# Performance work log

Hardware: AMD Instinct MI355X
Metric: run time of the kernel (lower is better)

The kernel has to match this reference:

```python
import jax, jax.numpy as jnp
import numpy as np

N, D, E = 16384, 256, 8
H = D // 2  # gate hidden


def setup_inputs() -> dict:
    key = jax.random.key(0)
    ks = jax.random.split(key, 10)
    s = lambda fan_in: 1.0 / np.sqrt(fan_in)
    return {
        "x":   jax.random.normal(ks[0], (N, D), dtype=jnp.float32),
        # gate: Linear(D, D//2) -> ReLU -> Linear(D//2, E) -> Softmax
        "Wg1": jax.random.uniform(ks[1], (D, H), jnp.float32, -s(D), s(D)),
        "bg1": jax.random.uniform(ks[2], (H,), jnp.float32, -s(D), s(D)),
        "Wg2": jax.random.uniform(ks[3], (H, E), jnp.float32, -s(H), s(H)),
        "bg2": jax.random.uniform(ks[4], (E,), jnp.float32, -s(H), s(H)),
        # experts: per-expert Linear(D,D) -> ReLU -> (Dropout eval=identity) -> Linear(D,D)
        "W1": jax.random.uniform(ks[5], (E, D, D), jnp.float32, -s(D), s(D)),
        "b1": jax.random.uniform(ks[6], (E, D), jnp.float32, -s(D), s(D)),
        "W2": jax.random.uniform(ks[7], (E, D, D), jnp.float32, -s(D), s(D)),
        "b2": jax.random.uniform(ks[8], (E, D), jnp.float32, -s(D), s(D)),
    }


def reference(x, Wg1, bg1, Wg2, bg2, W1, b1, W2, b2):
    # gate: [N, E] softmax over experts
    g = jax.nn.softmax(jax.nn.relu(x @ Wg1 + bg1) @ Wg2 + bg2, axis=-1)
    # all experts applied densely via batched GEMMs (fuses the Python loop)
    h = jax.nn.relu(jnp.einsum("nd,edh->neh", x, W1) + b1)  # [N, E, D]
    y = jnp.einsum("neh,ehd->ned", h, W2) + b2              # [N, E, D]
    # weighted combine: sum_e g[n,e] * y[n,e,:]
    return jnp.einsum("ned,ne->nd", y, g)
```

## Files before the change

kernel.cpp:

```cpp
#include <hip/hip_runtime.h>


typedef unsigned short USH;
typedef float f32x4 __attribute__((ext_vector_type(4)));
typedef __bf16 bf16x8 __attribute__((ext_vector_type(8)));

#define AS1 __attribute__((address_space(1)))
#define AS3 __attribute__((address_space(3)))

__device__ __forceinline__ USH f2bf(float f) {
  unsigned int u = __float_as_uint(f);
  u += 0x7fffu + ((u >> 16) & 1u);
  return (USH)(u >> 16);
}

__device__ __forceinline__ void gl2lds16(const void* g, void* l) {
  __builtin_amdgcn_global_load_lds((AS1 const void*)g, (AS3 void*)l, 16, 0, 0);
}


__global__ __launch_bounds__(256) void k_prep(
    const float* __restrict__ x,
    const float* __restrict__ Wg1,
    const float* __restrict__ W1,
    const float* __restrict__ W2,
    USH* __restrict__ xb, USH* __restrict__ wg1t,
    USH* __restrict__ w1f, USH* __restrict__ w2f) {
  __shared__ float T[64][65];
  int b = blockIdx.x, tid = threadIdx.x;

  if (b < 2048) {
    size_t i8 = ((size_t)b * 256 + tid) * 8;
    float4 a = *(const float4*)(x + i8);
    float4 c = *(const float4*)(x + i8 + 4);
    USH v[8];
    v[0] = f2bf(a.x); v[1] = f2bf(a.y); v[2] = f2bf(a.z); v[3] = f2bf(a.w);
    v[4] = f2bf(c.x); v[5] = f2bf(c.y); v[6] = f2bf(c.z); v[7] = f2bf(c.w);
    *(uint4*)(xb + i8) = *(const uint4*)v;
  } else if (b < 2176) {
    int bp = b - 2048;
    int e = bp >> 4, tl = bp & 15;
    int c0 = (tl >> 2) * 64, h0 = (tl & 3) * 64;
    const float* src = W1 + (size_t)e * 65536;
#pragma unroll
    for (int p = 0; p < 4; ++p) {
      int r = p * 16 + (tid >> 4), d4 = (tid & 15) * 4;
      float4 v = *(const float4*)(src + (size_t)(c0 + r) * 256 + h0 + d4);
      T[r][d4] = v.x; T[r][d4 + 1] = v.y; T[r][d4 + 2] = v.z; T[r][d4 + 3] = v.w;
    }
    __syncthreads();
#pragma unroll
    for (int p = 0; p < 4; ++p) {
      int hr = p * 16 + (tid >> 4), c4 = (tid & 15) * 4;
      USH w[4];
#pragma unroll
      for (int j = 0; j < 4; ++j) w[j] = f2bf(T[c4 + j][hr]);
      int h = h0 + hr;
      int t = h >> 4, lh = h & 15;
      int kt = c0 >> 6, ch = c4 >> 5, q = (c4 >> 3) & 3, u0 = c4 & 7;
      size_t idx = ((size_t)((e * 64 + kt * 16 + t) * 2 + ch)) * 512 + (q * 16 + lh) * 8 + u0;
      *(uint2*)(w1f + idx) = *(const uint2*)w;
    }
  } else if (b < 2184) {
    int bp = b - 2176;
    int c0 = (bp >> 1) * 64, h0 = (bp & 1) * 64;
#pragma unroll
    for (int p = 0; p < 4; ++p) {
      int r = p * 16 + (tid >> 4), d4 = (tid & 15) * 4;
      float4 v = *(const float4*)(Wg1 + (size_t)(c0 + r) * 128 + h0 + d4);
      T[r][d4] = v.x; T[r][d4 + 1] = v.y; T[r][d4 + 2] = v.z; T[r][d4 + 3] = v.w;
    }
    __syncthreads();
#pragma unroll
    for (int p = 0; p < 4; ++p) {
      int hr = p * 16 + (tid >> 4), c4 = (tid & 15) * 4;
      USH w[4];
#pragma unroll
      for (int j = 0; j < 4; ++j) w[j] = f2bf(T[c4 + j][hr]);
      *(uint2*)(wg1t + (size_t)(h0 + hr) * 256 + c0 + c4) = *(const uint2*)w;
    }
  } else {
    int bp = b - 2184;
    int e = bp >> 4, tl = bp & 15;
    int h0 = (tl >> 2) * 64, d0 = (tl & 3) * 64;
    const float* src = W2 + (size_t)e * 65536;
#pragma unroll
    for (int p = 0; p < 4; ++p) {
      int r = p * 16 + (tid >> 4), d4 = (tid & 15) * 4;
      float4 v = *(const float4*)(src + (size_t)(h0 + r) * 256 + d0 + d4);
      T[r][d4] = v.x; T[r][d4 + 1] = v.y; T[r][d4 + 2] = v.z; T[r][d4 + 3] = v.w;
    }
    __syncthreads();
#pragma unroll
    for (int p = 0; p < 4; ++p) {
      int dr = p * 16 + (tid >> 4), h4 = (tid & 15) * 4;
      USH w[4];
#pragma unroll
      for (int j = 0; j < 4; ++j) w[j] = f2bf(T[h4 + j][dr]);
      int d = d0 + dr;
      int t = d >> 4, ld = d & 15;
      int ht = h0 >> 6, ch = h4 >> 5, q = (h4 >> 3) & 3, u0 = h4 & 7;
      size_t idx = ((size_t)((e * 64 + ht * 16 + t) * 2 + ch)) * 512 + (q * 16 + ld) * 8 + u0;
      *(uint2*)(w2f + idx) = *(const uint2*)w;
    }
  }
}


__global__ __launch_bounds__(256) void k_gate(const USH* __restrict__ xb,
                                              const USH* __restrict__ wg1t,
                                              const float* __restrict__ bg1,
                                              const float* __restrict__ wg2,
                                              const float* __restrict__ bg2,
                                              float* __restrict__ g) {
  __shared__ __align__(16) USH As[32 * 64];
  __shared__ __align__(16) USH Bs[128 * 64];
  __shared__ float hg[32 * 129];
  __shared__ float bg1s[128];
  __shared__ float w2s[128 * 8];
  __shared__ float b2s[8];
  __shared__ float lg[32 * 8];

  int tid = threadIdx.x;
  int wave = tid >> 6, lane = tid & 63;
  int quad = lane >> 4, l16 = lane & 15;
  int sw = l16 & 7;
  int wr = wave >> 1, wc = wave & 1;
  int rowBase = blockIdx.x * 32;

  for (int t = tid; t < 1024; t += 256) w2s[t] = wg2[t];
  if (tid < 8) b2s[tid] = bg2[tid];
  if (tid < 128) bg1s[tid] = bg1[tid];

  f32x4 acc[4] = {};
  for (int kt = 0; kt < 4; ++kt) {
    int kb = kt * 64;
    {
      int r = tid >> 3, c8 = (tid & 7) ^ (r & 7);
      gl2lds16(xb + (size_t)(rowBase + r) * 256 + kb + c8 * 8, As + (size_t)tid * 8);
    }
#pragma unroll
    for (int c = 0; c < 4; ++c) {
      int i = c * 256 + tid;
      int r = i >> 3, c8 = (i & 7) ^ (r & 7);
      gl2lds16(wg1t + (size_t)r * 256 + kb + c8 * 8, Bs + (size_t)i * 8);
    }
    __syncthreads();
#pragma unroll
    for (int kkc = 0; kkc < 8; kkc += 4) {
      bf16x8 av = *(const bf16x8*)(As + (wr * 16 + l16) * 64 + (((kkc + quad) ^ sw) * 8));
#pragma unroll
      for (int j = 0; j < 4; ++j) {
        bf16x8 bv = *(const bf16x8*)(Bs + (wc * 64 + j * 16 + l16) * 64 + (((kkc + quad) ^ sw) * 8));
        acc[j] = __builtin_amdgcn_mfma_f32_16x16x32_bf16(av, bv, acc[j], 0, 0, 0);
      }
    }
    __syncthreads();
  }

#pragma unroll
  for (int j = 0; j < 4; ++j)
#pragma unroll
    for (int r = 0; r < 4; ++r) {
      int row = wr * 16 + quad * 4 + r;
      int col = wc * 64 + j * 16 + l16;
      hg[row * 129 + col] = fmaxf(acc[j][r] + bg1s[col], 0.0f);
    }
  __syncthreads();

  {
    int row = tid >> 3, p = tid & 7;
    float s = b2s[p];
    for (int k = 0; k < 128; ++k) s += hg[row * 129 + k] * w2s[k * 8 + p];
    lg[row * 8 + p] = s;
  }
  __syncthreads();

  if (tid < 32) {
    float l[8];
    float m = -1e30f;
#pragma unroll
    for (int e = 0; e < 8; ++e) { l[e] = lg[tid * 8 + e]; m = fmaxf(m, l[e]); }
    float s = 0.0f;
#pragma unroll
    for (int e = 0; e < 8; ++e) { l[e] = expf(l[e] - m); s += l[e]; }
    float inv = 1.0f / s;
    size_t grow = rowBase + tid;
#pragma unroll
    for (int e = 0; e < 8; ++e) g[grow * 8 + e] = l[e] * inv;
  }
}


__global__ __launch_bounds__(512, 2) void k_moe(const USH* __restrict__ xb,
                                                const USH* __restrict__ w1f,
                                                const USH* __restrict__ w2f,
                                                const float* __restrict__ b1,
                                                const float* __restrict__ b2,
                                                const float* __restrict__ g,
                                                float* __restrict__ out) {
  __shared__ __align__(16) USH Hs[64 * 256];
  __shared__ float b1s[2048];
  __shared__ float b2s[2048];
  __shared__ float gs[512];

  int tid = threadIdx.x;
  int wave = tid >> 6, lane = tid & 63;
  int quad = lane >> 4, l16 = lane & 15;
  int sw = l16 & 7;
  int rowBase = blockIdx.x * 64;

#pragma unroll
  for (int t = 0; t < 4; ++t) {
    b1s[t * 512 + tid] = b1[t * 512 + tid];
    b2s[t * 512 + tid] = b2[t * 512 + tid];
  }
  gs[tid] = g[(size_t)rowBase * 8 + tid];

  bf16x8 xr[4][2][4];
#pragma unroll
  for (int kt = 0; kt < 4; ++kt)
#pragma unroll
    for (int c = 0; c < 2; ++c)
#pragma unroll
      for (int j = 0; j < 4; ++j)
        xr[kt][c][j] = *(const bf16x8*)(xb + (size_t)(rowBase + j * 16 + l16) * 256 +
                                        kt * 64 + c * 32 + quad * 8);

  __syncthreads();

  f32x4 oacc[4][2] = {};

#pragma unroll 1
  for (int e = 0; e < 8; ++e) {
    const USH* W1e = w1f + (size_t)e * 65536;
    const USH* W2e = w2f + (size_t)e * 65536;
    f32x4 hacc[2][4] = {};

#pragma unroll
    for (int kt = 0; kt < 4; ++kt)
#pragma unroll
      for (int c = 0; c < 2; ++c) {
        bf16x8 av[2];
#pragma unroll
        for (int i = 0; i < 2; ++i)
          av[i] = *(const bf16x8*)(W1e + (size_t)((kt * 16 + wave * 2 + i) * 2 + c) * 512 + lane * 8);
#pragma unroll
        for (int i = 0; i < 2; ++i)
#pragma unroll
          for (int j = 0; j < 4; ++j)
            hacc[i][j] = __builtin_amdgcn_mfma_f32_16x16x32_bf16(av[i], xr[kt][c][j], hacc[i][j], 0, 0, 0);
      }

#pragma unroll
    for (int i = 0; i < 2; ++i) {
      int slot = (wave & 1) * 4 + i * 2 + (quad >> 1);
      int hb = wave * 32 + i * 16 + quad * 4;
#pragma unroll
      for (int j = 0; j < 4; ++j) {
        int n = j * 16 + l16;
        float gg = gs[n * 8 + e];
        USH w4[4];
#pragma unroll
        for (int r = 0; r < 4; ++r)
          w4[r] = f2bf(fmaxf(hacc[i][j][r] + b1s[e * 256 + hb + r], 0.0f) * gg);
        int off = n * 256 + (wave >> 1) * 64 + ((slot ^ (n & 7)) * 8) + (quad & 1) * 4;
        *(uint2*)(Hs + off) = *(const uint2*)w4;
      }
    }
    __syncthreads();

#pragma unroll
    for (int ht = 0; ht < 4; ++ht)
#pragma unroll
      for (int c = 0; c < 2; ++c) {
        bf16x8 bv[2], av[4];
#pragma unroll
        for (int j = 0; j < 2; ++j)
          bv[j] = *(const bf16x8*)(W2e + (size_t)((ht * 16 + wave * 2 + j) * 2 + c) * 512 + lane * 8);
#pragma unroll
        for (int i = 0; i < 4; ++i)
          av[i] = *(const bf16x8*)(Hs + (i * 16 + l16) * 256 + ht * 64 + (((c * 4 + quad) ^ sw) * 8));
#pragma unroll
        for (int i = 0; i < 4; ++i)
#pragma unroll
          for (int j = 0; j < 2; ++j)
            oacc[i][j] = __builtin_amdgcn_mfma_f32_16x16x32_bf16(av[i], bv[j], oacc[i][j], 0, 0, 0);
      }
    __syncthreads();
  }

#pragma unroll
  for (int i = 0; i < 4; ++i)
#pragma unroll
    for (int r = 0; r < 4; ++r) {
      int n = i * 16 + quad * 4 + r;
      const float* gr = gs + n * 8;
      size_t grow = (size_t)(rowBase + n) * 256;
#pragma unroll
      for (int j = 0; j < 2; ++j) {
        int d = wave * 32 + j * 16 + l16;
        float bias = 0.0f;
#pragma unroll
        for (int ee = 0; ee < 8; ++ee) bias += gr[ee] * b2s[ee * 256 + d];
        out[grow + d] = oacc[i][j][r] + bias;
      }
    }
}


extern "C" void kernel_launch(void* const* d_in, const int* in_sizes, int n_in,
                              void* d_out, int out_size, void* d_ws, size_t ws_size,
                              hipStream_t stream) {
  const float* x   = (const float*)d_in[0];
  const float* Wg1 = (const float*)d_in[1];
  const float* bg1 = (const float*)d_in[2];
  const float* Wg2 = (const float*)d_in[3];
  const float* bg2 = (const float*)d_in[4];
  const float* W1  = (const float*)d_in[5];
  const float* b1  = (const float*)d_in[6];
  const float* W2  = (const float*)d_in[7];
  const float* b2  = (const float*)d_in[8];
  float* out = (float*)d_out;

  char* ws = (char*)d_ws;
  USH*   xb  = (USH*)(ws);
  USH*   w1f = (USH*)(ws + 8388608);
  USH*   wg1t = (USH*)(ws + 9437184);
  USH*   w2f = (USH*)(ws + 9502720);
  float* g   = (float*)(ws + 10584064);

  hipLaunchKernelGGL(k_prep, dim3(2312), dim3(256), 0, stream,
                     x, Wg1, W1, W2, xb, wg1t, w1f, w2f);
  hipLaunchKernelGGL(k_gate, dim3(512), dim3(256), 0, stream,
                     xb, wg1t, bg1, Wg2, bg2, g);
  hipLaunchKernelGGL(k_moe, dim3(256), dim3(512), 0, stream,
                     xb, w1f, w2f, b1, b2, g, out);
}
```

Before: 145.8 us.

## Software-pipeline expert weight loads and double-buffer hidden tile in MoE kernel

```diff
diff --git a/kernel.cpp b/kernel.cpp
--- a/kernel.cpp
+++ b/kernel.cpp
@@ -192,17 +192,18 @@
 }
 
 
-__global__ __launch_bounds__(512, 2) void k_moe(const USH* __restrict__ xb,
-                                                const USH* __restrict__ w1f,
-                                                const USH* __restrict__ w2f,
-                                                const float* __restrict__ b1,
-                                                const float* __restrict__ b2,
-                                                const float* __restrict__ g,
-                                                float* __restrict__ out) {
-  __shared__ __align__(16) USH Hs[64 * 256];
+__global__ __launch_bounds__(512) void k_moe(const USH* __restrict__ xb,
+                                             const USH* __restrict__ w1f,
+                                             const USH* __restrict__ w2f,
+                                             const float* __restrict__ b1,
+                                             const float* __restrict__ b2,
+                                             const float* __restrict__ g,
+                                             float* __restrict__ out) {
+  __shared__ __align__(16) USH xs[4 * 64 * 64];
+  __shared__ __align__(16) USH Hs[2][64 * 256];
   __shared__ float b1s[2048];
   __shared__ float b2s[2048];
-  __shared__ float gs[512];
+  __shared__ float gse[512];
 
   int tid = threadIdx.x;
   int wave = tid >> 6, lane = tid & 63;
@@ -211,47 +212,85 @@
   int rowBase = blockIdx.x * 64;
 
 #pragma unroll
+  for (int it = 0; it < 4; ++it) {
+    int i = it * 512 + tid;
+    int kt = i >> 9, rem = i & 511;
+    int r = rem >> 3, slot = rem & 7;
+    int c8 = slot ^ (r & 7);
+    gl2lds16(xb + (size_t)(rowBase + r) * 256 + kt * 64 + c8 * 8, xs + (size_t)i * 8);
+  }
+
+  bf16x8 wra[8], wrb[8];
+  auto LDWH = [&](bf16x8* dst, const USH* We, int tb) {
+#pragma unroll
+    for (int k = 0; k < 2; ++k)
+#pragma unroll
+      for (int c = 0; c < 2; ++c)
+#pragma unroll
+        for (int i = 0; i < 2; ++i)
+          dst[k * 4 + c * 2 + i] = *(const bf16x8*)(
+              We + (size_t)(((tb + k) * 16 + wave * 2 + i) * 2 + c) * 512 + lane * 8);
+  };
+  LDWH(wra, w1f, 0);
+  LDWH(wrb, w1f, 2);
+
+#pragma unroll
   for (int t = 0; t < 4; ++t) {
     b1s[t * 512 + tid] = b1[t * 512 + tid];
     b2s[t * 512 + tid] = b2[t * 512 + tid];
   }
-  gs[tid] = g[(size_t)rowBase * 8 + tid];
-
-  bf16x8 xr[4][2][4];
-#pragma unroll
-  for (int kt = 0; kt < 4; ++kt)
-#pragma unroll
-    for (int c = 0; c < 2; ++c)
-#pragma unroll
-      for (int j = 0; j < 4; ++j)
-        xr[kt][c][j] = *(const bf16x8*)(xb + (size_t)(rowBase + j * 16 + l16) * 256 +
-                                        kt * 64 + c * 32 + quad * 8);
-
-  __syncthreads();
+  {
+    int e = tid >> 6, n = tid & 63;
+    gse[tid] = g[(size_t)(rowBase + n) * 8 + e];
+  }
+
+  asm volatile("s_waitcnt vmcnt(0) lgkmcnt(0)" ::: "memory");
+  __builtin_amdgcn_s_barrier();
 
   f32x4 oacc[4][2] = {};
 
 #pragma unroll 1
   for (int e = 0; e < 8; ++e) {
-    const USH* W1e = w1f + (size_t)e * 65536;
     const USH* W2e = w2f + (size_t)e * 65536;
+    const USH* W1n = w1f + (size_t)((e + 1) & 7) * 65536;
     f32x4 hacc[2][4] = {};
 
 #pragma unroll
-    for (int kt = 0; kt < 4; ++kt)
+    for (int kt = 0; kt < 2; ++kt)
 #pragma unroll
       for (int c = 0; c < 2; ++c) {
-        bf16x8 av[2];
+        int cs = ((c * 4 + quad) ^ sw) * 8;
+        bf16x8 bv[4];
+#pragma unroll
+        for (int j = 0; j < 4; ++j)
+          bv[j] = *(const bf16x8*)(xs + kt * 4096 + (j * 16 + l16) * 64 + cs);
 #pragma unroll
         for (int i = 0; i < 2; ++i)
-          av[i] = *(const bf16x8*)(W1e + (size_t)((kt * 16 + wave * 2 + i) * 2 + c) * 512 + lane * 8);
+#pragma unroll
+          for (int j = 0; j < 4; ++j)
+            hacc[i][j] = __builtin_amdgcn_mfma_f32_16x16x32_bf16(
+                wra[kt * 4 + c * 2 + i], bv[j], hacc[i][j], 0, 0, 0);
+      }
+    LDWH(wra, W2e, 0);
+#pragma unroll
+    for (int kt = 2; kt < 4; ++kt)
+#pragma unroll
+      for (int c = 0; c < 2; ++c) {
+        int cs = ((c * 4 + quad) ^ sw) * 8;
+        bf16x8 bv[4];
+#pragma unroll
+        for (int j = 0; j < 4; ++j)
+          bv[j] = *(const bf16x8*)(xs + kt * 4096 + (j * 16 + l16) * 64 + cs);
 #pragma unroll
         for (int i = 0; i < 2; ++i)
 #pragma unroll
           for (int j = 0; j < 4; ++j)
-            hacc[i][j] = __builtin_amdgcn_mfma_f32_16x16x32_bf16(av[i], xr[kt][c][j], hacc[i][j], 0, 0, 0);
-      }
-
+            hacc[i][j] = __builtin_amdgcn_mfma_f32_16x16x32_bf16(
+                wrb[(kt - 2) * 4 + c * 2 + i], bv[j], hacc[i][j], 0, 0, 0);
+      }
+    LDWH(wrb, W2e, 2);
+
+    USH* Hb = &Hs[e & 1][0];
 #pragma unroll
     for (int i = 0; i < 2; ++i) {
       int slot = (wave & 1) * 4 + i * 2 + (quad >> 1);
@@ -259,35 +298,53 @@
 #pragma unroll
       for (int j = 0; j < 4; ++j) {
         int n = j * 16 + l16;
-        float gg = gs[n * 8 + e];
+        float gg = gse[e * 64 + n];
         USH w4[4];
 #pragma unroll
         for (int r = 0; r < 4; ++r)
           w4[r] = f2bf(fmaxf(hacc[i][j][r] + b1s[e * 256 + hb + r], 0.0f) * gg);
         int off = n * 256 + (wave >> 1) * 64 + ((slot ^ (n & 7)) * 8) + (quad & 1) * 4;
-        *(uint2*)(Hs + off) = *(const uint2*)w4;
-      }
-    }
-    __syncthreads();
-
-#pragma unroll
-    for (int ht = 0; ht < 4; ++ht)
+        *(uint2*)(Hb + off) = *(const uint2*)w4;
+      }
+    }
+
+    asm volatile("s_waitcnt lgkmcnt(0)" ::: "memory");
+    __builtin_amdgcn_s_barrier();
+
+#pragma unroll
+    for (int ht = 0; ht < 2; ++ht)
 #pragma unroll
       for (int c = 0; c < 2; ++c) {
-        bf16x8 bv[2], av[4];
-#pragma unroll
-        for (int j = 0; j < 2; ++j)
-          bv[j] = *(const bf16x8*)(W2e + (size_t)((ht * 16 + wave * 2 + j) * 2 + c) * 512 + lane * 8);
+        int cs = ((c * 4 + quad) ^ sw) * 8;
+        bf16x8 av[4];
 #pragma unroll
         for (int i = 0; i < 4; ++i)
-          av[i] = *(const bf16x8*)(Hs + (i * 16 + l16) * 256 + ht * 64 + (((c * 4 + quad) ^ sw) * 8));
+          av[i] = *(const bf16x8*)(Hb + (i * 16 + l16) * 256 + ht * 64 + cs);
 #pragma unroll
         for (int i = 0; i < 4; ++i)
 #pragma unroll
           for (int j = 0; j < 2; ++j)
-            oacc[i][j] = __builtin_amdgcn_mfma_f32_16x16x32_bf16(av[i], bv[j], oacc[i][j], 0, 0, 0);
-      }
-    __syncthreads();
+            oacc[i][j] = __builtin_amdgcn_mfma_f32_16x16x32_bf16(
+                av[i], wra[ht * 4 + c * 2 + j], oacc[i][j], 0, 0, 0);
+      }
+    LDWH(wra, W1n, 0);
+#pragma unroll
+    for (int ht = 2; ht < 4; ++ht)
+#pragma unroll
+      for (int c = 0; c < 2; ++c) {
+        int cs = ((c * 4 + quad) ^ sw) * 8;
+        bf16x8 av[4];
+#pragma unroll
+        for (int i = 0; i < 4; ++i)
+          av[i] = *(const bf16x8*)(Hb + (i * 16 + l16) * 256 + ht * 64 + cs);
+#pragma unroll
+        for (int i = 0; i < 4; ++i)
+#pragma unroll
+          for (int j = 0; j < 2; ++j)
+            oacc[i][j] = __builtin_amdgcn_mfma_f32_16x16x32_bf16(
+                av[i], wrb[(ht - 2) * 4 + c * 2 + j], oacc[i][j], 0, 0, 0);
+      }
+    LDWH(wrb, W1n, 2);
   }
 
 #pragma unroll
@@ -295,14 +352,13 @@
 #pragma unroll
     for (int r = 0; r < 4; ++r) {
       int n = i * 16 + quad * 4 + r;
-      const float* gr = gs + n * 8;
       size_t grow = (size_t)(rowBase + n) * 256;
 #pragma unroll
       for (int j = 0; j < 2; ++j) {
         int d = wave * 32 + j * 16 + l16;
         float bias = 0.0f;
 #pragma unroll
-        for (int ee = 0; ee < 8; ++ee) bias += gr[ee] * b2s[ee * 256 + d];
+        for (int ee = 0; ee < 8; ++ee) bias += gse[ee * 64 + n] * b2s[ee * 256 + d];
         out[grow + d] = oacc[i][j][r] + bias;
       }
     }
```

New measurement: 130.6 us. -10.4%, faster.
